# Performance work log

Measured on AMD Instinct MI355X. Metric: run time of the kernel, lower is better.

The kernel has to match this reference:

```python
import jax, jax.numpy as jnp
import numpy as np


def setup_inputs() -> dict:
    key = jax.random.key(0)
    B, C, H, W = 8, 64, 64, 64
    x = jax.random.normal(key, (B, C, H, W), dtype=jnp.float32)
    return {"x": x}


def reference(x) -> jnp.ndarray:
    # x: (B, C, H, W). Spatial self-attention over N = H*W positions with
    # Q = K = V = flattened x, no scaling, no projections (the Conv2d in the
    # original __init__ is never used in forward).
    B, C, H, W = x.shape
    N = H * W
    f = x.reshape(B, C, N)  # (B, C, N)
    # att[b, n, m] = sum_c f[b, c, n] * f[b, c, m]  -> (B, N, N)
    att = jnp.einsum('bcn,bcm->bnm', f, f)
    att = jax.nn.softmax(att, axis=-1)
    # outp[b, c, n] = sum_m f[b, c, m] * att[b, n, m]^T  (f_x @ att)
    outp = jnp.einsum('bcm,bmn->bcn', f, att).reshape(B, C, H, W)
    return x + outp
```

## Files before the change

### kernel.cpp

```cpp
#include <hip/hip_runtime.h>

typedef short v8s __attribute__((ext_vector_type(8)));
typedef short v4s __attribute__((ext_vector_type(4)));
typedef float v4f __attribute__((ext_vector_type(4)));

#define LOG2E 1.44269504088896340736f

#define WS_FBF_T 0u
#define WS_FBF   4194304u
#define WS_G     8388608u
#define WS_BMAX  8519680u
#define WS_NEED  8521728u

__device__ __forceinline__ unsigned short f2bf_rne(float f) {
  unsigned int u = __builtin_bit_cast(unsigned int, f);
  u += 0x7FFFu + ((u >> 16) & 1u);
  return (unsigned short)(u >> 16);
}

__device__ __forceinline__ unsigned int pack_hi16(float hi, float lo) {
#if defined(__has_builtin) && __has_builtin(__builtin_amdgcn_perm)
  return __builtin_amdgcn_perm(__builtin_bit_cast(unsigned int, hi),
                               __builtin_bit_cast(unsigned int, lo), 0x07060302u);
#else
  return (__builtin_bit_cast(unsigned int, hi) & 0xFFFF0000u) |
         (__builtin_bit_cast(unsigned int, lo) >> 16);
#endif
}

__global__ __launch_bounds__(256) void prep_kernel(
    const float* __restrict__ x, unsigned short* __restrict__ fbf_t,
    unsigned short* __restrict__ fbf, float* __restrict__ g, float* __restrict__ bmax) {
  __shared__ float red[128];
  __shared__ float wmax[2];
  const int t = threadIdx.x;
  const int b = blockIdx.x & 7, nch = blockIdx.x >> 3;
  const int n = (nch << 7) + (t & 127);
  const int chalf = t >> 7, c0 = chalf << 5;

  const float* xb = x + (((size_t)(b * 64 + c0)) << 12) + n;
  unsigned short* fb = fbf + (((size_t)(b * 64 + c0)) << 12) + n;
  float sq = 0.f;
  unsigned int pk[16];
#pragma unroll
  for (int cc = 0; cc < 16; ++cc) {
    float v0 = xb[(size_t)(2 * cc) << 12];
    float v1 = xb[(size_t)(2 * cc + 1) << 12];
    sq = __builtin_fmaf(v0, v0, sq);
    sq = __builtin_fmaf(v1, v1, sq);
    unsigned short w0 = f2bf_rne(v0), w1 = f2bf_rne(v1);
    pk[cc] = (unsigned int)w0 | ((unsigned int)w1 << 16);
    fb[(size_t)(2 * cc) << 12] = w0;
    fb[(size_t)(2 * cc + 1) << 12] = w1;
  }
  unsigned short* ft = fbf_t + ((size_t)b << 18) + (size_t)n * 64 + c0;
#pragma unroll
  for (int k = 0; k < 4; ++k) {
    uint4 u = make_uint4(pk[4 * k], pk[4 * k + 1], pk[4 * k + 2], pk[4 * k + 3]);
    *(uint4*)(ft + k * 8) = u;
  }
  if (chalf == 0) red[t] = sq;
  __syncthreads();
  if (chalf == 1) {
    float tot = sq + red[t & 127];
    g[b * 4096 + n] = tot;
    float m = tot;
    m = fmaxf(m, __shfl_xor(m, 1, 64));
    m = fmaxf(m, __shfl_xor(m, 2, 64));
    m = fmaxf(m, __shfl_xor(m, 4, 64));
    m = fmaxf(m, __shfl_xor(m, 8, 64));
    m = fmaxf(m, __shfl_xor(m, 16, 64));
    m = fmaxf(m, __shfl_xor(m, 32, 64));
    if ((t & 63) == 0) wmax[(t >> 6) & 1] = m;
  }
  __syncthreads();
  if (t == 0) bmax[b * 32 + nch] = fmaxf(wmax[0], wmax[1]);
}

__global__ __launch_bounds__(1024) void chanattn_main(
    const float* __restrict__ x, const unsigned short* __restrict__ fbf_t,
    const unsigned short* __restrict__ fbf, const float* __restrict__ g,
    const float* __restrict__ bmax, float* __restrict__ out) {
  __shared__ __align__(16) unsigned char smem[73728];
  unsigned short* sKtB = (unsigned short*)smem;
  unsigned short* sVcB = (unsigned short*)(smem + 18432);
  float* lred = (float*)(smem + 71680);
  const int BUF = 17920;

  const int tid = threadIdx.x;
  const int wave = tid >> 6, lane = tid & 63, quad = lane >> 4, l15 = lane & 15;
  const int qg = wave >> 2, kg = wave & 3;
  const int b = blockIdx.x & 7, qt = blockIdx.x >> 3;

  const unsigned short* fT = fbf_t + ((size_t)b << 18);
  const unsigned short* fV = fbf + ((size_t)b << 18);

  const int sKey = tid >> 3, sC = (tid & 7) << 3;
  const int vC = tid >> 4, vK = (tid & 15) << 3;
  const int vSlot = (vK & ~31) + ((vK & 8) ? 16 : 0) + ((vK & 16) ? 4 : 0);

  float gm = bmax[b * 32 + (lane & 31)];
  gm = fmaxf(gm, __shfl_xor(gm, 1, 64));
  gm = fmaxf(gm, __shfl_xor(gm, 2, 64));
  gm = fmaxf(gm, __shfl_xor(gm, 4, 64));
  gm = fmaxf(gm, __shfl_xor(gm, 8, 64));
  gm = fmaxf(gm, __shfl_xor(gm, 16, 64));
  float gq[2];
#pragma unroll
  for (int jq = 0; jq < 2; ++jq)
    gq[jq] = g[b * 4096 + qt * 128 + qg * 32 + jq * 16 + l15];

  *(v8s*)&sKtB[sKey * 72 + sC] =
      *(const v8s*)&fT[(size_t)(qt * 128 + sKey) * 64 + sC];
  v8s pfk = *(const v8s*)&fT[(size_t)sKey * 64 + sC];
  v8s pfv = *(const v8s*)&fV[(size_t)vC * 4096 + vK];

  __syncthreads();
  v8s bQ[2][2];
#pragma unroll
  for (int jq = 0; jq < 2; ++jq)
#pragma unroll
    for (int cs = 0; cs < 2; ++cs)
      bQ[jq][cs] = *(const v8s*)&sKtB[(qg * 32 + jq * 16 + l15) * 72 + cs * 32 + quad * 8];
  float msc[2];
#pragma unroll
  for (int jq = 0; jq < 2; ++jq) msc[jq] = __builtin_sqrtf(gq[jq] * gm) * LOG2E;
  __syncthreads();

  *(v8s*)&sKtB[sKey * 72 + sC] = pfk;
  {
    v4s lo, hi;
#pragma unroll
    for (int j = 0; j < 4; ++j) { lo[j] = pfv[j]; hi[j] = pfv[j + 4]; }
    *(v4s*)&sVcB[vC * 136 + vSlot] = lo;
    *(v4s*)&sVcB[vC * 136 + vSlot + 8] = hi;
  }
  pfk = *(const v8s*)&fT[(size_t)(128 + sKey) * 64 + sC];
  pfv = *(const v8s*)&fV[(size_t)vC * 4096 + 128 + vK];

  v4f oacc[4][2];
  float rsum[2];
#pragma unroll
  for (int ct = 0; ct < 4; ++ct)
#pragma unroll
    for (int jq = 0; jq < 2; ++jq) oacc[ct][jq] = (v4f){0.f, 0.f, 0.f, 0.f};
  rsum[0] = 0.f; rsum[1] = 0.f;

  for (int kt = 0; kt < 32; ++kt) {
    __syncthreads();
    const int po = (kt & 1) * BUF;
    const int pn = ((kt & 1) ^ 1) * BUF;

    v8s aK[2][2];
#pragma unroll
    for (int t = 0; t < 2; ++t)
#pragma unroll
      for (int cs = 0; cs < 2; ++cs)
        aK[t][cs] =
            *(const v8s*)&sKtB[po + (kg * 32 + t * 16 + l15) * 72 + cs * 32 + quad * 8];
    v8s aV[4];
#pragma unroll
    for (int ct = 0; ct < 4; ++ct)
      aV[ct] = *(const v8s*)&sVcB[po + (ct * 16 + l15) * 136 + kg * 32 + quad * 8];

    {
      const int jq = 0;
      v4f s0 = (v4f){0.f, 0.f, 0.f, 0.f}, s1 = (v4f){0.f, 0.f, 0.f, 0.f};
#pragma unroll
      for (int cs = 0; cs < 2; ++cs) {
        s0 = __builtin_amdgcn_mfma_f32_16x16x32_bf16(aK[0][cs], bQ[jq][cs], s0, 0, 0, 0);
        s1 = __builtin_amdgcn_mfma_f32_16x16x32_bf16(aK[1][cs], bQ[jq][cs], s1, 0, 0, 0);
      }
      float p0[4], p1[4];
#pragma unroll
      for (int r = 0; r < 4; ++r) {
        p0[r] = __builtin_amdgcn_exp2f(__builtin_fmaf(s0[r], LOG2E, -msc[jq]));
        p1[r] = __builtin_amdgcn_exp2f(__builtin_fmaf(s1[r], LOG2E, -msc[jq]));
      }
      rsum[jq] += ((p0[0] + p0[1]) + (p0[2] + p0[3])) +
                  ((p1[0] + p1[1]) + (p1[2] + p1[3]));
      uint4 up;
      up.x = pack_hi16(p0[1], p0[0]);
      up.y = pack_hi16(p0[3], p0[2]);
      up.z = pack_hi16(p1[1], p1[0]);
      up.w = pack_hi16(p1[3], p1[2]);
      v8s bp = __builtin_bit_cast(v8s, up);
#pragma unroll
      for (int ct = 0; ct < 4; ++ct)
        oacc[ct][jq] =
            __builtin_amdgcn_mfma_f32_16x16x32_bf16(aV[ct], bp, oacc[ct][jq], 0, 0, 0);
    }

    if (kt < 31) {
      *(v8s*)&sKtB[pn + sKey * 72 + sC] = pfk;
      v4s lo, hi;
#pragma unroll
      for (int j = 0; j < 4; ++j) { lo[j] = pfv[j]; hi[j] = pfv[j + 4]; }
      *(v4s*)&sVcB[pn + vC * 136 + vSlot] = lo;
      *(v4s*)&sVcB[pn + vC * 136 + vSlot + 8] = hi;
    }
    if (kt < 30) {
      const int k0 = (kt + 2) << 7;
      pfk = *(const v8s*)&fT[(size_t)(k0 + sKey) * 64 + sC];
      pfv = *(const v8s*)&fV[(size_t)vC * 4096 + k0 + vK];
    }

    {
      const int jq = 1;
      v4f s0 = (v4f){0.f, 0.f, 0.f, 0.f}, s1 = (v4f){0.f, 0.f, 0.f, 0.f};
#pragma unroll
      for (int cs = 0; cs < 2; ++cs) {
        s0 = __builtin_amdgcn_mfma_f32_16x16x32_bf16(aK[0][cs], bQ[jq][cs], s0, 0, 0, 0);
        s1 = __builtin_amdgcn_mfma_f32_16x16x32_bf16(aK[1][cs], bQ[jq][cs], s1, 0, 0, 0);
      }
      float p0[4], p1[4];
#pragma unroll
      for (int r = 0; r < 4; ++r) {
        p0[r] = __builtin_amdgcn_exp2f(__builtin_fmaf(s0[r], LOG2E, -msc[jq]));
        p1[r] = __builtin_amdgcn_exp2f(__builtin_fmaf(s1[r], LOG2E, -msc[jq]));
      }
      rsum[jq] += ((p0[0] + p0[1]) + (p0[2] + p0[3])) +
                  ((p1[0] + p1[1]) + (p1[2] + p1[3]));
      uint4 up;
      up.x = pack_hi16(p0[1], p0[0]);
      up.y = pack_hi16(p0[3], p0[2]);
      up.z = pack_hi16(p1[1], p1[0]);
      up.w = pack_hi16(p1[3], p1[2]);
      v8s bp = __builtin_bit_cast(v8s, up);
#pragma unroll
      for (int ct = 0; ct < 4; ++ct)
        oacc[ct][jq] =
            __builtin_amdgcn_mfma_f32_16x16x32_bf16(aV[ct], bp, oacc[ct][jq], 0, 0, 0);
    }
  }

#pragma unroll
  for (int jq = 0; jq < 2; ++jq) {
    float s = rsum[jq];
    s += __shfl_xor(s, 16, 64);
    s += __shfl_xor(s, 32, 64);
    rsum[jq] = s;
  }
  if (quad == 0) {
#pragma unroll
    for (int jq = 0; jq < 2; ++jq)
      lred[(qg * 32 + jq * 16 + l15) * 4 + kg] = rsum[jq];
  }
  __syncthreads();
  float inv[2];
#pragma unroll
  for (int jq = 0; jq < 2; ++jq) {
    const float4 lv = *(const float4*)&lred[(qg * 32 + jq * 16 + l15) * 4];
    inv[jq] = __builtin_amdgcn_rcpf((lv.x + lv.y) + (lv.z + lv.w));
  }

  float* Obuf = (float*)smem;
#pragma unroll
  for (int round = 0; round < 4; ++round) {
    if (kg == round) {
#pragma unroll
      for (int ct = 0; ct < 4; ++ct)
#pragma unroll
        for (int jq = 0; jq < 2; ++jq)
#pragma unroll
          for (int r = 0; r < 4; ++r) {
            float val = oacc[ct][jq][r] * inv[jq];
            float* p = &Obuf[(ct * 16 + quad * 4 + r) * 132 + qg * 32 + jq * 16 + l15];
            if (round == 0) *p = val; else *p += val;
          }
    }
    __syncthreads();
  }
#pragma unroll
  for (int j = 0; j < 2; ++j) {
    int idx = tid + j * 1024;
    int c = idx >> 5, q4 = idx & 31;
    const float4 o = *(const float4*)&Obuf[c * 132 + q4 * 4];
    size_t gidx = ((size_t)(b * 64 + c) << 12) + (unsigned)(qt * 128 + q4 * 4);
    const float4 xv = *(const float4*)(x + gidx);
    float4 rv;
    rv.x = xv.x + o.x; rv.y = xv.y + o.y; rv.z = xv.z + o.z; rv.w = xv.w + o.w;
    *(float4*)(out + gidx) = rv;
  }
}

__global__ __launch_bounds__(512) void
chanattn_fallback(const float* __restrict__ x, float* __restrict__ out) {
  __shared__ __align__(16) unsigned char smem[54272];
  unsigned short* sKt = (unsigned short*)smem;
  unsigned short* sVc = (unsigned short*)(smem + 18432);
  unsigned short* sP  = (unsigned short*)(smem + 35840);
  const int tid = threadIdx.x;
  const int wave = tid >> 6, lane = tid & 63, quad = lane >> 4, l15 = lane & 15;
  const int b = blockIdx.x & 7, qt = blockIdx.x >> 3;
  const float* fb = x + (size_t)b * (64 * 4096);
  const int skey = tid & 127, sc0 = (tid >> 7) << 4;
  {
    float vq[16];
#pragma unroll
    for (int j = 0; j < 16; ++j) vq[j] = fb[(sc0 + j) * 4096 + qt * 128 + skey];
    unsigned short us[16];
#pragma unroll
    for (int j = 0; j < 16; ++j) us[j] = f2bf_rne(vq[j]);
#pragma unroll
    for (int h = 0; h < 2; ++h) {
      v8s t;
#pragma unroll
      for (int j = 0; j < 8; ++j) t[j] = (short)us[h * 8 + j];
      *(v8s*)&sKt[skey * 72 + sc0 + h * 8] = t;
    }
  }
  float vk[16];
#pragma unroll
  for (int j = 0; j < 16; ++j) vk[j] = fb[(sc0 + j) * 4096 + skey];
  __syncthreads();
  v8s aq[2];
#pragma unroll
  for (int cs = 0; cs < 2; ++cs)
    aq[cs] = *(const v8s*)&sKt[(wave * 16 + l15) * 72 + cs * 32 + quad * 8];
  __syncthreads();
  v4f oacc[4];
#pragma unroll
  for (int ct = 0; ct < 4; ++ct) oacc[ct] = (v4f){0.f, 0.f, 0.f, 0.f};
  float m_run[4], l_run[4];
#pragma unroll
  for (int r = 0; r < 4; ++r) { m_run[r] = -3.0e38f; l_run[r] = 0.f; }
  unsigned short* sPw = sP + wave * (16 * 72);
  for (int kt = 0; kt < 32; ++kt) {
    {
      unsigned short us[16];
#pragma unroll
      for (int j = 0; j < 16; ++j) us[j] = f2bf_rne(vk[j]);
#pragma unroll
      for (int h = 0; h < 2; ++h) {
        v8s t;
#pragma unroll
        for (int j = 0; j < 8; ++j) t[j] = (short)us[h * 8 + j];
        *(v8s*)&sKt[skey * 72 + sc0 + h * 8] = t;
      }
#pragma unroll
      for (int j = 0; j < 16; ++j) sVc[(sc0 + j) * 136 + skey] = us[j];
    }
    __syncthreads();
    if (kt + 1 < 32) {
      const int m0 = (kt + 1) * 128;
#pragma unroll
      for (int j = 0; j < 16; ++j) vk[j] = fb[(sc0 + j) * 4096 + m0 + skey];
    }
    v4f sacc[8];
#pragma unroll
    for (int t = 0; t < 8; ++t) {
      v4f acc = (v4f){0.f, 0.f, 0.f, 0.f};
#pragma unroll
      for (int cs = 0; cs < 2; ++cs) {
        v8s bf = *(const v8s*)&sKt[(t * 16 + l15) * 72 + cs * 32 + quad * 8];
        acc = __builtin_amdgcn_mfma_f32_16x16x32_bf16(aq[cs], bf, acc, 0, 0, 0);
      }
      sacc[t] = acc;
    }
    float alpha[4], msc[4], rsum[4];
#pragma unroll
    for (int r = 0; r < 4; ++r) {
      float mv = sacc[0][r];
#pragma unroll
      for (int t = 1; t < 8; ++t) mv = fmaxf(mv, sacc[t][r]);
      mv = fmaxf(mv, __shfl_xor(mv, 8, 64));
      mv = fmaxf(mv, __shfl_xor(mv, 4, 64));
      mv = fmaxf(mv, __shfl_xor(mv, 2, 64));
      mv = fmaxf(mv, __shfl_xor(mv, 1, 64));
      float mnew = fmaxf(m_run[r], mv);
      alpha[r] = __builtin_amdgcn_exp2f((m_run[r] - mnew) * LOG2E);
      m_run[r] = mnew;
      msc[r] = mnew * LOG2E;
      l_run[r] *= alpha[r];
      rsum[r] = 0.f;
    }
#pragma unroll
    for (int ct = 0; ct < 4; ++ct)
#pragma unroll
      for (int r = 0; r < 4; ++r) oacc[ct][r] *= alpha[r];
#pragma unroll
    for (int half = 0; half < 2; ++half) {
#pragma unroll
      for (int t = half * 4; t < half * 4 + 4; ++t)
#pragma unroll
        for (int r = 0; r < 4; ++r) {
          float p = __builtin_amdgcn_exp2f(__builtin_fmaf(sacc[t][r], LOG2E, -msc[r]));
          rsum[r] += p;
          sPw[(quad * 4 + r) * 72 + (t - half * 4) * 16 + l15] = f2bf_rne(p);
        }
      asm volatile("s_waitcnt lgkmcnt(0)" ::: "memory");
#pragma unroll
      for (int ms = 0; ms < 2; ++ms) {
        v8s af = *(const v8s*)&sPw[l15 * 72 + ms * 32 + quad * 8];
#pragma unroll
        for (int ct = 0; ct < 4; ++ct) {
          v8s bf = *(const v8s*)&sVc[(ct * 16 + l15) * 136 + (half * 2 + ms) * 32 + quad * 8];
          oacc[ct] = __builtin_amdgcn_mfma_f32_16x16x32_bf16(af, bf, oacc[ct], 0, 0, 0);
        }
      }
      asm volatile("s_waitcnt lgkmcnt(0)" ::: "memory");
    }
#pragma unroll
    for (int r = 0; r < 4; ++r) {
      float s = rsum[r];
      s += __shfl_xor(s, 8, 64);
      s += __shfl_xor(s, 4, 64);
      s += __shfl_xor(s, 2, 64);
      s += __shfl_xor(s, 1, 64);
      l_run[r] += s;
    }
    __syncthreads();
  }
  float inv[4];
#pragma unroll
  for (int r = 0; r < 4; ++r) inv[r] = __builtin_amdgcn_rcpf(l_run[r]);
  float* sOt = (float*)smem;
#pragma unroll
  for (int ct = 0; ct < 4; ++ct)
#pragma unroll
    for (int r = 0; r < 4; ++r)
      sOt[(ct * 16 + l15) * 132 + wave * 16 + quad * 4 + r] = oacc[ct][r] * inv[r];
  __syncthreads();
#pragma unroll
  for (int j = 0; j < 4; ++j) {
    int idx = tid + j * 512;
    int nv = idx & 31, c = idx >> 5;
    float4 o = *(const float4*)&sOt[c * 132 + nv * 4];
    size_t gaddr = (size_t)b * (64 * 4096) + (size_t)c * 4096 + (size_t)(qt * 128 + nv * 4);
    float4 xv = *(const float4*)(x + gaddr);
    float4 res = make_float4(xv.x + o.x, xv.y + o.y, xv.z + o.z, xv.w + o.w);
    *(float4*)(out + gaddr) = res;
  }
}

extern "C" void kernel_launch(void* const* d_in, const int* in_sizes, int n_in,
                              void* d_out, int out_size, void* d_ws, size_t ws_size,
                              hipStream_t stream) {
  const float* xin = (const float*)d_in[0];
  float* out = (float*)d_out;
  if (ws_size >= (size_t)WS_NEED) {
    unsigned short* fbf_t = (unsigned short*)((char*)d_ws + WS_FBF_T);
    unsigned short* fbf = (unsigned short*)((char*)d_ws + WS_FBF);
    float* g = (float*)((char*)d_ws + WS_G);
    float* bmax = (float*)((char*)d_ws + WS_BMAX);
    prep_kernel<<<dim3(256), dim3(256), 0, stream>>>(xin, fbf_t, fbf, g, bmax);
    chanattn_main<<<dim3(256), dim3(1024), 0, stream>>>(xin, fbf_t, fbf, g, bmax, out);
  } else {
    chanattn_fallback<<<dim3(256), dim3(512), 0, stream>>>(xin, out);
  }
}
```

Measured before the change: 106.5 us.

## Drop LDS staging; load K/V fragments directly from global in pre-permuted layout

The main kernel no longer stages K and V tiles through double-buffered shared memory. Each wave now reads its MFMA operand fragments straight from global memory (served mostly from L2), using a V copy that prep writes already permuted into MFMA slot order. Blocks shrink to 256 threads, each covering 64 queries, with 512 blocks and a 3-blocks-per-CU launch bound. This removes the per-iteration barriers and LDS traffic, but every wave now issues its own global loads, and K/V are read redundantly across waves and blocks.

```diff
diff --git a/kernel.cpp b/kernel.cpp
--- a/kernel.cpp
+++ b/kernel.cpp
@@ -1,13 +1,12 @@
 #include <hip/hip_runtime.h>
 
 typedef short v8s __attribute__((ext_vector_type(8)));
-typedef short v4s __attribute__((ext_vector_type(4)));
 typedef float v4f __attribute__((ext_vector_type(4)));
 
 #define LOG2E 1.44269504088896340736f
 
 #define WS_FBF_T 0u
-#define WS_FBF   4194304u
+#define WS_FVP   4194304u
 #define WS_G     8388608u
 #define WS_BMAX  8519680u
 #define WS_NEED  8521728u
@@ -30,40 +29,38 @@
 
 __global__ __launch_bounds__(256) void prep_kernel(
     const float* __restrict__ x, unsigned short* __restrict__ fbf_t,
-    unsigned short* __restrict__ fbf, float* __restrict__ g, float* __restrict__ bmax) {
-  __shared__ float red[128];
-  __shared__ float wmax[2];
+    unsigned short* __restrict__ fvp, float* __restrict__ g, float* __restrict__ bmax) {
+  __shared__ float red[4][64];
   const int t = threadIdx.x;
-  const int b = blockIdx.x & 7, nch = blockIdx.x >> 3;
-  const int n = (nch << 7) + (t & 127);
-  const int chalf = t >> 7, c0 = chalf << 5;
-
-  const float* xb = x + (((size_t)(b * 64 + c0)) << 12) + n;
-  unsigned short* fb = fbf + (((size_t)(b * 64 + c0)) << 12) + n;
+  const int b = blockIdx.x & 7, ch = blockIdx.x >> 3;
+  const int n0 = ch << 6, nn = t & 63, n = n0 + nn, cg = t >> 6;
+
+  const int kin = nn & 31;
+  const int slot = (kin < 16) ? (((kin >> 2) << 3) + (kin & 3))
+                              : ((((kin - 16) >> 2) << 3) + ((kin - 16) & 3) + 4);
+  const int ncol = (n & ~31) + slot;
+
   float sq = 0.f;
-  unsigned int pk[16];
-#pragma unroll
-  for (int cc = 0; cc < 16; ++cc) {
-    float v0 = xb[(size_t)(2 * cc) << 12];
-    float v1 = xb[(size_t)(2 * cc + 1) << 12];
-    sq = __builtin_fmaf(v0, v0, sq);
-    sq = __builtin_fmaf(v1, v1, sq);
-    unsigned short w0 = f2bf_rne(v0), w1 = f2bf_rne(v1);
-    pk[cc] = (unsigned int)w0 | ((unsigned int)w1 << 16);
-    fb[(size_t)(2 * cc) << 12] = w0;
-    fb[(size_t)(2 * cc + 1) << 12] = w1;
-  }
-  unsigned short* ft = fbf_t + ((size_t)b << 18) + (size_t)n * 64 + c0;
-#pragma unroll
-  for (int k = 0; k < 4; ++k) {
-    uint4 u = make_uint4(pk[4 * k], pk[4 * k + 1], pk[4 * k + 2], pk[4 * k + 3]);
-    *(uint4*)(ft + k * 8) = u;
-  }
-  if (chalf == 0) red[t] = sq;
-  __syncthreads();
-  if (chalf == 1) {
-    float tot = sq + red[t & 127];
-    g[b * 4096 + n] = tot;
+  unsigned short w[16];
+#pragma unroll
+  for (int j = 0; j < 16; ++j) {
+    const int c = cg * 16 + j;
+    float v = x[((size_t)(b * 64 + c) << 12) + n];
+    sq = __builtin_fmaf(v, v, sq);
+    w[j] = f2bf_rne(v);
+  }
+  unsigned short* ft = fbf_t + ((size_t)b << 18) + (size_t)n * 64 + cg * 16;
+  *(v8s*)ft = *(v8s*)&w[0];
+  *(v8s*)(ft + 8) = *(v8s*)&w[8];
+#pragma unroll
+  for (int j = 0; j < 16; ++j)
+    fvp[((size_t)(b * 64 + cg * 16 + j) << 12) + ncol] = w[j];
+
+  red[cg][nn] = sq;
+  __syncthreads();
+  if (t < 64) {
+    float tot = (red[0][t] + red[1][t]) + (red[2][t] + red[3][t]);
+    g[b * 4096 + n0 + t] = tot;
     float m = tot;
     m = fmaxf(m, __shfl_xor(m, 1, 64));
     m = fmaxf(m, __shfl_xor(m, 2, 64));
@@ -71,100 +68,83 @@
     m = fmaxf(m, __shfl_xor(m, 8, 64));
     m = fmaxf(m, __shfl_xor(m, 16, 64));
     m = fmaxf(m, __shfl_xor(m, 32, 64));
-    if ((t & 63) == 0) wmax[(t >> 6) & 1] = m;
-  }
-  __syncthreads();
-  if (t == 0) bmax[b * 32 + nch] = fmaxf(wmax[0], wmax[1]);
-}
-
-__global__ __launch_bounds__(1024) void chanattn_main(
+    if (t == 0) bmax[b * 64 + ch] = m;
+  }
+}
+
+__global__ __launch_bounds__(256, 3) void chanattn_main(
     const float* __restrict__ x, const unsigned short* __restrict__ fbf_t,
-    const unsigned short* __restrict__ fbf, const float* __restrict__ g,
+    const unsigned short* __restrict__ fvp, const float* __restrict__ g,
     const float* __restrict__ bmax, float* __restrict__ out) {
-  __shared__ __align__(16) unsigned char smem[73728];
-  unsigned short* sKtB = (unsigned short*)smem;
-  unsigned short* sVcB = (unsigned short*)(smem + 18432);
-  float* lred = (float*)(smem + 71680);
-  const int BUF = 17920;
+  __shared__ __align__(16) unsigned char smem[18432];
+  float* Obuf = (float*)smem;
+  float* lred = (float*)(smem + 17408);
 
   const int tid = threadIdx.x;
-  const int wave = tid >> 6, lane = tid & 63, quad = lane >> 4, l15 = lane & 15;
-  const int qg = wave >> 2, kg = wave & 3;
-  const int b = blockIdx.x & 7, qt = blockIdx.x >> 3;
+  const int kg = tid >> 6, lane = tid & 63, quad = lane >> 4, l15 = lane & 15;
+  const int b = blockIdx.x & 7, q64 = blockIdx.x >> 3;
 
   const unsigned short* fT = fbf_t + ((size_t)b << 18);
-  const unsigned short* fV = fbf + ((size_t)b << 18);
-
-  const int sKey = tid >> 3, sC = (tid & 7) << 3;
-  const int vC = tid >> 4, vK = (tid & 15) << 3;
-  const int vSlot = (vK & ~31) + ((vK & 8) ? 16 : 0) + ((vK & 16) ? 4 : 0);
-
-  float gm = bmax[b * 32 + (lane & 31)];
+  const unsigned short* fV = fvp + ((size_t)b << 18);
+
+  v8s bQ[4][2];
+#pragma unroll
+  for (int jq = 0; jq < 4; ++jq)
+#pragma unroll
+    for (int cs = 0; cs < 2; ++cs)
+      bQ[jq][cs] = *(const v8s*)&fT[(size_t)(q64 * 64 + jq * 16 + l15) * 64 + cs * 32 + quad * 8];
+
+  float gm = bmax[b * 64 + lane];
   gm = fmaxf(gm, __shfl_xor(gm, 1, 64));
   gm = fmaxf(gm, __shfl_xor(gm, 2, 64));
   gm = fmaxf(gm, __shfl_xor(gm, 4, 64));
   gm = fmaxf(gm, __shfl_xor(gm, 8, 64));
   gm = fmaxf(gm, __shfl_xor(gm, 16, 64));
-  float gq[2];
-#pragma unroll
-  for (int jq = 0; jq < 2; ++jq)
-    gq[jq] = g[b * 4096 + qt * 128 + qg * 32 + jq * 16 + l15];
-
-  *(v8s*)&sKtB[sKey * 72 + sC] =
-      *(const v8s*)&fT[(size_t)(qt * 128 + sKey) * 64 + sC];
-  v8s pfk = *(const v8s*)&fT[(size_t)sKey * 64 + sC];
-  v8s pfv = *(const v8s*)&fV[(size_t)vC * 4096 + vK];
-
-  __syncthreads();
-  v8s bQ[2][2];
-#pragma unroll
-  for (int jq = 0; jq < 2; ++jq)
+  gm = fmaxf(gm, __shfl_xor(gm, 32, 64));
+  float msc[4];
+#pragma unroll
+  for (int jq = 0; jq < 4; ++jq)
+    msc[jq] = __builtin_sqrtf(g[b * 4096 + q64 * 64 + jq * 16 + l15] * gm) * LOG2E;
+
+  const int kbase = (kg * 32 + l15) * 64 + quad * 8;
+  int vbase[4];
+#pragma unroll
+  for (int ct = 0; ct < 4; ++ct)
+    vbase[ct] = (ct * 16 + l15) * 4096 + kg * 32 + quad * 8;
+
+  v8s aK[2][2];
+#pragma unroll
+  for (int t = 0; t < 2; ++t)
 #pragma unroll
     for (int cs = 0; cs < 2; ++cs)
-      bQ[jq][cs] = *(const v8s*)&sKtB[(qg * 32 + jq * 16 + l15) * 72 + cs * 32 + quad * 8];
-  float msc[2];
-#pragma unroll
-  for (int jq = 0; jq < 2; ++jq) msc[jq] = __builtin_sqrtf(gq[jq] * gm) * LOG2E;
-  __syncthreads();
-
-  *(v8s*)&sKtB[sKey * 72 + sC] = pfk;
-  {
-    v4s lo, hi;
-#pragma unroll
-    for (int j = 0; j < 4; ++j) { lo[j] = pfv[j]; hi[j] = pfv[j + 4]; }
-    *(v4s*)&sVcB[vC * 136 + vSlot] = lo;
-    *(v4s*)&sVcB[vC * 136 + vSlot + 8] = hi;
-  }
-  pfk = *(const v8s*)&fT[(size_t)(128 + sKey) * 64 + sC];
-  pfv = *(const v8s*)&fV[(size_t)vC * 4096 + 128 + vK];
-
-  v4f oacc[4][2];
-  float rsum[2];
+      aK[t][cs] = *(const v8s*)&fT[kbase + t * 1024 + cs * 32];
+
+  v4f oacc[4][4];
+  float rsum[4];
 #pragma unroll
   for (int ct = 0; ct < 4; ++ct)
 #pragma unroll
-    for (int jq = 0; jq < 2; ++jq) oacc[ct][jq] = (v4f){0.f, 0.f, 0.f, 0.f};
-  rsum[0] = 0.f; rsum[1] = 0.f;
+    for (int jq = 0; jq < 4; ++jq) oacc[ct][jq] = (v4f){0.f, 0.f, 0.f, 0.f};
+#pragma unroll
+  for (int jq = 0; jq < 4; ++jq) rsum[jq] = 0.f;
 
   for (int kt = 0; kt < 32; ++kt) {
-    __syncthreads();
-    const int po = (kt & 1) * BUF;
-    const int pn = ((kt & 1) ^ 1) * BUF;
-
-    v8s aK[2][2];
-#pragma unroll
-    for (int t = 0; t < 2; ++t)
-#pragma unroll
-      for (int cs = 0; cs < 2; ++cs)
-        aK[t][cs] =
-            *(const v8s*)&sKtB[po + (kg * 32 + t * 16 + l15) * 72 + cs * 32 + quad * 8];
+    const int k0 = kt << 7;
     v8s aV[4];
 #pragma unroll
     for (int ct = 0; ct < 4; ++ct)
-      aV[ct] = *(const v8s*)&sVcB[po + (ct * 16 + l15) * 136 + kg * 32 + quad * 8];
-
-    {
-      const int jq = 0;
+      aV[ct] = *(const v8s*)&fV[vbase[ct] + k0];
+    v8s aKn[2][2];
+    if (kt < 31) {
+#pragma unroll
+      for (int t = 0; t < 2; ++t)
+#pragma unroll
+        for (int cs = 0; cs < 2; ++cs)
+          aKn[t][cs] = *(const v8s*)&fT[kbase + (k0 + 128) * 64 + t * 1024 + cs * 32];
+    }
+
+#pragma unroll
+    for (int jq = 0; jq < 4; ++jq) {
       v4f s0 = (v4f){0.f, 0.f, 0.f, 0.f}, s1 = (v4f){0.f, 0.f, 0.f, 0.f};
 #pragma unroll
       for (int cs = 0; cs < 2; ++cs) {
@@ -190,52 +170,16 @@
         oacc[ct][jq] =
             __builtin_amdgcn_mfma_f32_16x16x32_bf16(aV[ct], bp, oacc[ct][jq], 0, 0, 0);
     }
-
     if (kt < 31) {
-      *(v8s*)&sKtB[pn + sKey * 72 + sC] = pfk;
-      v4s lo, hi;
-#pragma unroll
-      for (int j = 0; j < 4; ++j) { lo[j] = pfv[j]; hi[j] = pfv[j + 4]; }
-      *(v4s*)&sVcB[pn + vC * 136 + vSlot] = lo;
-      *(v4s*)&sVcB[pn + vC * 136 + vSlot + 8] = hi;
-    }
-    if (kt < 30) {
-      const int k0 = (kt + 2) << 7;
-      pfk = *(const v8s*)&fT[(size_t)(k0 + sKey) * 64 + sC];
-      pfv = *(const v8s*)&fV[(size_t)vC * 4096 + k0 + vK];
-    }
-
-    {
-      const int jq = 1;
-      v4f s0 = (v4f){0.f, 0.f, 0.f, 0.f}, s1 = (v4f){0.f, 0.f, 0.f, 0.f};
-#pragma unroll
-      for (int cs = 0; cs < 2; ++cs) {
-        s0 = __builtin_amdgcn_mfma_f32_16x16x32_bf16(aK[0][cs], bQ[jq][cs], s0, 0, 0, 0);
-        s1 = __builtin_amdgcn_mfma_f32_16x16x32_bf16(aK[1][cs], bQ[jq][cs], s1, 0, 0, 0);
-      }
-      float p0[4], p1[4];
-#pragma unroll
-      for (int r = 0; r < 4; ++r) {
-        p0[r] = __builtin_amdgcn_exp2f(__builtin_fmaf(s0[r], LOG2E, -msc[jq]));
-        p1[r] = __builtin_amdgcn_exp2f(__builtin_fmaf(s1[r], LOG2E, -msc[jq]));
-      }
-      rsum[jq] += ((p0[0] + p0[1]) + (p0[2] + p0[3])) +
-                  ((p1[0] + p1[1]) + (p1[2] + p1[3]));
-      uint4 up;
-      up.x = pack_hi16(p0[1], p0[0]);
-      up.y = pack_hi16(p0[3], p0[2]);
-      up.z = pack_hi16(p1[1], p1[0]);
-      up.w = pack_hi16(p1[3], p1[2]);
-      v8s bp = __builtin_bit_cast(v8s, up);
-#pragma unroll
-      for (int ct = 0; ct < 4; ++ct)
-        oacc[ct][jq] =
-            __builtin_amdgcn_mfma_f32_16x16x32_bf16(aV[ct], bp, oacc[ct][jq], 0, 0, 0);
-    }
-  }
-
-#pragma unroll
-  for (int jq = 0; jq < 2; ++jq) {
+#pragma unroll
+      for (int t = 0; t < 2; ++t)
+#pragma unroll
+        for (int cs = 0; cs < 2; ++cs) aK[t][cs] = aKn[t][cs];
+    }
+  }
+
+#pragma unroll
+  for (int jq = 0; jq < 4; ++jq) {
     float s = rsum[jq];
     s += __shfl_xor(s, 16, 64);
     s += __shfl_xor(s, 32, 64);
@@ -243,40 +187,39 @@
   }
   if (quad == 0) {
 #pragma unroll
-    for (int jq = 0; jq < 2; ++jq)
-      lred[(qg * 32 + jq * 16 + l15) * 4 + kg] = rsum[jq];
-  }
-  __syncthreads();
-  float inv[2];
-#pragma unroll
-  for (int jq = 0; jq < 2; ++jq) {
-    const float4 lv = *(const float4*)&lred[(qg * 32 + jq * 16 + l15) * 4];
+    for (int jq = 0; jq < 4; ++jq)
+      lred[(jq * 16 + l15) * 4 + kg] = rsum[jq];
+  }
+  __syncthreads();
+  float inv[4];
+#pragma unroll
+  for (int jq = 0; jq < 4; ++jq) {
+    const float4 lv = *(const float4*)&lred[(jq * 16 + l15) * 4];
     inv[jq] = __builtin_amdgcn_rcpf((lv.x + lv.y) + (lv.z + lv.w));
   }
 
-  float* Obuf = (float*)smem;
 #pragma unroll
   for (int round = 0; round < 4; ++round) {
     if (kg == round) {
 #pragma unroll
       for (int ct = 0; ct < 4; ++ct)
 #pragma unroll
-        for (int jq = 0; jq < 2; ++jq)
+        for (int jq = 0; jq < 4; ++jq)
 #pragma unroll
           for (int r = 0; r < 4; ++r) {
             float val = oacc[ct][jq][r] * inv[jq];
-            float* p = &Obuf[(ct * 16 + quad * 4 + r) * 132 + qg * 32 + jq * 16 + l15];
+            float* p = &Obuf[(ct * 16 + quad * 4 + r) * 68 + jq * 16 + l15];
             if (round == 0) *p = val; else *p += val;
           }
     }
     __syncthreads();
   }
 #pragma unroll
-  for (int j = 0; j < 2; ++j) {
-    int idx = tid + j * 1024;
-    int c = idx >> 5, q4 = idx & 31;
-    const float4 o = *(const float4*)&Obuf[c * 132 + q4 * 4];
-    size_t gidx = ((size_t)(b * 64 + c) << 12) + (unsigned)(qt * 128 + q4 * 4);
+  for (int j = 0; j < 4; ++j) {
+    int idx = tid + j * 256;
+    int c = idx >> 4, q4 = idx & 15;
+    const float4 o = *(const float4*)&Obuf[c * 68 + q4 * 4];
+    size_t gidx = ((size_t)(b * 64 + c) << 12) + (unsigned)(q64 * 64 + q4 * 4);
     const float4 xv = *(const float4*)(x + gidx);
     float4 rv;
     rv.x = xv.x + o.x; rv.y = xv.y + o.y; rv.z = xv.z + o.z; rv.w = xv.w + o.w;
@@ -441,11 +384,11 @@
   float* out = (float*)d_out;
   if (ws_size >= (size_t)WS_NEED) {
     unsigned short* fbf_t = (unsigned short*)((char*)d_ws + WS_FBF_T);
-    unsigned short* fbf = (unsigned short*)((char*)d_ws + WS_FBF);
+    unsigned short* fvp = (unsigned short*)((char*)d_ws + WS_FVP);
     float* g = (float*)((char*)d_ws + WS_G);
     float* bmax = (float*)((char*)d_ws + WS_BMAX);
-    prep_kernel<<<dim3(256), dim3(256), 0, stream>>>(xin, fbf_t, fbf, g, bmax);
-    chanattn_main<<<dim3(256), dim3(1024), 0, stream>>>(xin, fbf_t, fbf, g, bmax, out);
+    prep_kernel<<<dim3(512), dim3(256), 0, stream>>>(xin, fbf_t, fvp, g, bmax);
+    chanattn_main<<<dim3(512), dim3(256), 0, stream>>>(xin, fbf_t, fvp, g, bmax, out);
   } else {
     chanattn_fallback<<<dim3(256), dim3(512), 0, stream>>>(xin, out);
   }
```

After: 142.2 us. +33.5%, slower.
